# Kernel tuning notes

Measured on AMD Instinct MI355X. Metric: run time of the kernel, lower is better.

Reference implementation:

```python
import jax, jax.numpy as jnp
import numpy as np

B, S, D, H, L, TPB = 4, 1020, 1024, 16, 4, 17
VOBS, VACT = 4096, 16
DH = D // H
EPS = 1e-3  # keras LayerNormalization default epsilon


def _ln(x, g, b):
    m = jnp.mean(x, axis=-1, keepdims=True)
    v = jnp.mean((x - m) ** 2, axis=-1, keepdims=True)
    return (x - m) * jax.lax.rsqrt(v + EPS) * g + b


def setup_inputs() -> dict:
    key = jax.random.key(0)
    ks = iter(jax.random.split(key, 64))
    def p(shape, s=0.02):
        return jax.random.normal(next(ks), shape, jnp.float32) * s
    pos = np.arange(S)
    is_obs = jnp.asarray((pos % TPB) < (TPB - 1))
    tok = jax.random.randint(next(ks), (B, S), 0, VOBS)
    tok = jnp.where(is_obs[None, :], tok, tok % VACT).astype(jnp.int32)
    d = dict(
        tokens=tok,
        pos_emb=p((S, D)), emb_obs=p((VOBS, D)), emb_act=p((VACT, D)),
        ln1_g=jnp.ones((L, D)), ln1_b=jnp.zeros((L, D)),
        wq=p((L, D, D)), bq=jnp.zeros((L, D)),
        wk=p((L, D, D)), bk=jnp.zeros((L, D)),
        wv=p((L, D, D)), bv=jnp.zeros((L, D)),
        wo=p((L, D, D)), bo=jnp.zeros((L, D)),
        ln2_g=jnp.ones((L, D)), ln2_b=jnp.zeros((L, D)),
        w1=p((L, D, 4 * D)), b1=jnp.zeros((L, 4 * D)),
        w2=p((L, 4 * D, D)), b2=jnp.zeros((L, D)),
        lnf_g=jnp.ones((D,)), lnf_b=jnp.zeros((D,)),
        ho1=p((D, D)), bo1=jnp.zeros((D,)),
        ho2=p((D, VOBS)), bo2=jnp.zeros((VOBS,)),
        he1=p((D, D)), be1=jnp.zeros((D,)),
        he2=p((D, 2)), be2=jnp.zeros((2,)),
    )
    return d


def reference(tokens, pos_emb, emb_obs, emb_act, ln1_g, ln1_b, wq, bq, wk, bk,
              wv, bv, wo, bo, ln2_g, ln2_b, w1, b1, w2, b2, lnf_g, lnf_b,
              ho1, bo1, ho2, bo2, he1, be1, he2, be2):
    pos = jnp.arange(S)
    is_obs = (pos % TPB) < (TPB - 1)  # obs positions within each block
    # token embedding: obs table on obs positions, act table on act positions
    x = jnp.where(is_obs[None, :, None],
                  emb_obs[jnp.minimum(tokens, VOBS - 1)],
                  emb_act[jnp.minimum(tokens, VACT - 1)])
    x = x + pos_emb[None]
    neg_mask = (1.0 - jnp.tril(jnp.ones((S, S), jnp.float32))) * -1e9
    inv_sqrt_dk = 1.0 / np.sqrt(DH).astype(np.float32)
    for i in range(L):
        h = _ln(x, ln1_g[i], ln1_b[i])
        q = (h @ wq[i] + bq[i]).reshape(B, S, H, DH).transpose(0, 2, 1, 3)
        k = (h @ wk[i] + bk[i]).reshape(B, S, H, DH).transpose(0, 2, 1, 3)
        v = (h @ wv[i] + bv[i]).reshape(B, S, H, DH).transpose(0, 2, 1, 3)
        scores = jnp.einsum('bhqd,bhkd->bhqk', q, k) * inv_sqrt_dk + neg_mask
        w = jax.nn.softmax(scores, axis=-1)
        o = jnp.einsum('bhqk,bhkd->bhqd', w, v).transpose(0, 2, 1, 3).reshape(B, S, D)
        x = x + (o @ wo[i] + bo[i])
        h = _ln(x, ln2_g[i], ln2_b[i])
        h = jax.nn.gelu(h @ w1[i] + b1[i], approximate=False) @ w2[i] + b2[i]
        x = x + h
    x = _ln(x, lnf_g, lnf_b)
    # head slices (static)
    p_np = np.arange(S)
    head_obs_idx = jnp.asarray(np.nonzero(((p_np + 1) % TPB) != (TPB - 1))[0])  # 960
    act_idx = jnp.asarray(np.nonzero((p_np % TPB) == (TPB - 1))[0])            # 60
    xo = x[:, head_obs_idx]
    logits_obs = jax.nn.relu(xo @ ho1 + bo1) @ ho2 + bo2   # [B, 960, VOBS]
    xe = x[:, act_idx]
    logits_ends = jax.nn.relu(xe @ he1 + be1) @ he2 + be2  # [B, 60, 2]
    return (logits_obs, logits_ends)
```

## Files before the change

kernel.cpp:

```cpp
#include <hip/hip_runtime.h>
#include <hip/hip_bf16.h>
#include <math.h>

namespace {

constexpr int kS = 1020, kD = 1024, kTPB = 17, kDH = 64;
constexpr int kVOBS = 4096, kVACT = 16;
constexpr int kBS = 4080;
constexpr float kEPS = 1e-3f;

typedef float f32x4 __attribute__((ext_vector_type(4)));
typedef __bf16 bfx8 __attribute__((ext_vector_type(8)));
typedef unsigned short u16;
typedef u16 us8 __attribute__((ext_vector_type(8)));
typedef u16 us4 __attribute__((ext_vector_type(4)));

__device__ __forceinline__ float bf2f(u16 u) {
  union { unsigned int i; float f; } v; v.i = (unsigned int)u << 16; return v.f;
}
__device__ __forceinline__ u16 f2bf(float f) {
  union { float f; unsigned int i; } v; v.f = f;
  unsigned int r = v.i + 0x7FFFu + ((v.i >> 16) & 1u);
  return (u16)(r >> 16);
}

__global__ void k_embed(const int* __restrict__ tokens, const float* __restrict__ pos_emb,
                        const float* __restrict__ emb_obs, const float* __restrict__ emb_act,
                        float* __restrict__ x) {
  int bs = blockIdx.x;
  int s = bs % kS;
  int tk = tokens[bs];
  bool obs = (s % kTPB) < (kTPB - 1);
  const float* e;
  if (obs) { int t2 = tk < kVOBS - 1 ? tk : kVOBS - 1; e = emb_obs + (size_t)t2 * kD; }
  else     { int t2 = tk < kVACT - 1 ? tk : kVACT - 1; e = emb_act + (size_t)t2 * kD; }
  int c = threadIdx.x * 4;
  float4 ev = *(const float4*)(e + c);
  float4 pv = *(const float4*)(pos_emb + (size_t)s * kD + c);
  float4 o; o.x = ev.x + pv.x; o.y = ev.y + pv.y; o.z = ev.z + pv.z; o.w = ev.w + pv.w;
  *(float4*)(x + (size_t)bs * kD + c) = o;
}

__global__ void k_pack_bias(const float* __restrict__ bq, const float* __restrict__ bk,
                            const float* __restrict__ bv, float* __restrict__ bqkv) {
  int idx = blockIdx.x * 256 + threadIdx.x;
  int l = idx / 3072, rem = idx % 3072;
  int sel = rem >> 10, cc = rem & 1023;
  const float* src = sel == 0 ? bq : (sel == 1 ? bk : bv);
  bqkv[idx] = src[l * kD + cc];
}

__global__ void k_ln(const float* __restrict__ x, const float* __restrict__ g,
                     const float* __restrict__ b, u16* __restrict__ out) {
  int row = blockIdx.x;
  int t = threadIdx.x;
  const float* xr = x + (size_t)row * kD;
  float4 v = *(const float4*)(xr + t * 4);
  float s1 = v.x + v.y + v.z + v.w;
  float s2 = v.x * v.x + v.y * v.y + v.z * v.z + v.w * v.w;
  #pragma unroll
  for (int m = 32; m; m >>= 1) { s1 += __shfl_xor(s1, m); s2 += __shfl_xor(s2, m); }
  __shared__ float ls1[4], ls2[4];
  int w = t >> 6;
  if ((t & 63) == 0) { ls1[w] = s1; ls2[w] = s2; }
  __syncthreads();
  float S1 = ls1[0] + ls1[1] + ls1[2] + ls1[3];
  float S2 = ls2[0] + ls2[1] + ls2[2] + ls2[3];
  float mean = S1 * (1.0f / kD);
  float var = S2 * (1.0f / kD) - mean * mean;
  float rs = rsqrtf(var + kEPS);
  int c = t * 4;
  float4 gv = *(const float4*)(g + c);
  float4 bv = *(const float4*)(b + c);
  us4 o;
  o[0] = f2bf((v.x - mean) * rs * gv.x + bv.x);
  o[1] = f2bf((v.y - mean) * rs * gv.y + bv.y);
  o[2] = f2bf((v.z - mean) * rs * gv.z + bv.z);
  o[3] = f2bf((v.w - mean) * rs * gv.w + bv.w);
  *(us4*)(out + (size_t)row * kD + c) = o;
}

__global__ void k_transpose(const float* __restrict__ in, u16* __restrict__ out,
                            int R, int C, int ld) {
  __shared__ float tile[32][33];
  int tx = threadIdx.x, ty = threadIdx.y;
  int c0 = blockIdx.x * 32, r0 = blockIdx.y * 32;
  #pragma unroll
  for (int i = 0; i < 4; ++i)
    tile[ty + i * 8][tx] = in[(size_t)(r0 + ty + i * 8) * ld + c0 + tx];
  __syncthreads();
  #pragma unroll
  for (int i = 0; i < 4; ++i)
    out[(size_t)(c0 + ty + i * 8) * R + r0 + tx] = f2bf(tile[tx][ty + i * 8]);
}

struct T4 {
  const float* in0; const float* in1; const float* in2; const float* in3;
  u16* out0; u16* out1; u16* out2; u16* out3;
  int ld;
};
__global__ void k_transpose4(T4 sp) {
  const float* in; u16* out;
  switch (blockIdx.z) {
    case 0:  in = sp.in0; out = sp.out0; break;
    case 1:  in = sp.in1; out = sp.out1; break;
    case 2:  in = sp.in2; out = sp.out2; break;
    default: in = sp.in3; out = sp.out3; break;
  }
  __shared__ float tile[32][33];
  int tx = threadIdx.x, ty = threadIdx.y;
  int c0 = blockIdx.x * 32, r0 = blockIdx.y * 32;
  #pragma unroll
  for (int i = 0; i < 4; ++i)
    tile[ty + i * 8][tx] = in[(size_t)(r0 + ty + i * 8) * sp.ld + c0 + tx];
  __syncthreads();
  #pragma unroll
  for (int i = 0; i < 4; ++i)
    out[(size_t)(c0 + ty + i * 8) * 1024 + r0 + tx] = f2bf(tile[tx][ty + i * 8]);
}

template <int EPI, int BM>
__global__ void __launch_bounds__(256)
k_gemm(const u16* __restrict__ A, const u16* __restrict__ Bt, const float* __restrict__ bias,
       const float* __restrict__ resid, void* __restrict__ out, int M, int N, int K, int ldo) {
  constexpr int MFRAG = BM / 32;
  constexpr int LOADS = BM / 64 + 2;
  __shared__ alignas(16) u16 As[3][BM * 32];
  __shared__ alignas(16) u16 Bs[3][128 * 32];
  int tid = threadIdx.x;
  int m0 = blockIdx.x * BM, n0 = blockIdx.y * 128;
  int lane = tid & 63, wv = tid >> 6;
  int wm = wv >> 1, wn = wv & 1;
  f32x4 acc[MFRAG][4] = {};

  auto stage = [&](int buf, int k0) {
    #pragma unroll
    for (int n = 0; n < BM / 64; ++n) {
      int u = n * 256 + tid;
      int r = u >> 2, ch = u & 3;
      int gr = m0 + r; if (gr >= M) gr = M - 1;
      int cg = ch ^ ((r >> 1) & 3);
      const u16* src = A + (size_t)gr * K + k0 + cg * 8;
      __builtin_amdgcn_global_load_lds(
          (const __attribute__((address_space(1))) unsigned int*)src,
          (__attribute__((address_space(3))) unsigned int*)&As[buf][(n * 256 + wv * 64) * 8],
          16, 0, 0);
    }
    #pragma unroll
    for (int n = 0; n < 2; ++n) {
      int u = n * 256 + tid;
      int r = u >> 2, ch = u & 3;
      int cg = ch ^ ((r >> 1) & 3);
      const u16* src = Bt + (size_t)(n0 + r) * K + k0 + cg * 8;
      __builtin_amdgcn_global_load_lds(
          (const __attribute__((address_space(1))) unsigned int*)src,
          (__attribute__((address_space(3))) unsigned int*)&Bs[buf][(n * 256 + wv * 64) * 8],
          16, 0, 0);
    }
  };

  const int nk = K >> 5;
  stage(0, 0);
  stage(1, 32);
  stage(2, 64);
  for (int t = 0; t < nk; ++t) {
    int cur = t % 3;
    if (t + 2 < nk)
      asm volatile("s_waitcnt vmcnt(%0)" :: "i"(2 * LOADS) : "memory");
    else if (t + 1 < nk)
      asm volatile("s_waitcnt vmcnt(%0)" :: "i"(LOADS) : "memory");
    else
      asm volatile("s_waitcnt vmcnt(0)" ::: "memory");
    __builtin_amdgcn_s_barrier();
    __builtin_amdgcn_sched_barrier(0);

    bfx8 af[MFRAG], bfr[4];
    int ch = lane >> 4;
    #pragma unroll
    for (int mf = 0; mf < MFRAG; ++mf) {
      int row = wm * (BM / 2) + mf * 16 + (lane & 15);
      af[mf] = *(const bfx8*)(&As[cur][row * 32 + ((ch ^ ((row >> 1) & 3)) << 3)]);
    }
    #pragma unroll
    for (int nf = 0; nf < 4; ++nf) {
      int row = wn * 64 + nf * 16 + (lane & 15);
      bfr[nf] = *(const bfx8*)(&Bs[cur][row * 32 + ((ch ^ ((row >> 1) & 3)) << 3)]);
    }
    asm volatile("s_waitcnt lgkmcnt(0)" ::: "memory");
    __builtin_amdgcn_s_barrier();
    __builtin_amdgcn_sched_barrier(0);
    if (t + 3 < nk) stage(cur, (t + 3) << 5);

    #pragma unroll
    for (int mf = 0; mf < MFRAG; ++mf)
      #pragma unroll
      for (int nf = 0; nf < 4; ++nf)
        acc[mf][nf] = __builtin_amdgcn_mfma_f32_16x16x32_bf16(af[mf], bfr[nf], acc[mf][nf], 0, 0, 0);
  }

  #pragma unroll
  for (int mf = 0; mf < MFRAG; ++mf) {
    #pragma unroll
    for (int nf = 0; nf < 4; ++nf) {
      int gcol = n0 + wn * 64 + nf * 16 + (lane & 15);
      float bv = bias ? bias[gcol] : 0.0f;
      #pragma unroll
      for (int r = 0; r < 4; ++r) {
        int grow = m0 + wm * (BM / 2) + mf * 16 + (lane >> 4) * 4 + r;
        if (grow >= M) continue;
        float val = acc[mf][nf][r] + bv;
        size_t off2 = (size_t)grow * ldo + gcol;
        if (EPI == 0) {
          ((u16*)out)[off2] = f2bf(val);
        } else if (EPI == 1) {
          ((u16*)out)[off2] = f2bf(val > 0.f ? val : 0.f);
        } else if (EPI == 2) {
          ((u16*)out)[off2] = f2bf(0.5f * val * (1.f + erff(val * 0.70710678118654752440f)));
        } else if (EPI == 3) {
          ((float*)out)[off2] = resid[off2] + val;
        } else {
          ((float*)out)[off2] = val;
        }
      }
    }
  }
}

__device__ __forceinline__ int swz(int row, int colu16) {
  return (row * 64 + colu16) ^ ((row & 7) << 3) ^ ((row & 24) << 1);
}

__global__ void __launch_bounds__(256)
k_attn(const u16* __restrict__ q, const u16* __restrict__ k, const u16* __restrict__ v,
       u16* __restrict__ o, int ldin) {
  __shared__ u16 Kl[64 * 64];
  __shared__ u16 Vt[64 * 64];
  const int qb = blockIdx.x * 64;
  const int bh = blockIdx.y;
  const int b = bh >> 4, hh = bh & 15;
  const int tid = threadIdx.x;
  const int lane = tid & 63, w = tid >> 6;
  const int g = lane >> 4, c = lane & 15;
  const int q0 = qb + w * 16;
  const size_t base = (size_t)(b * kS) * ldin + hh * kDH;

  bfx8 qf0, qf1;
  {
    int qr = q0 + c; if (qr >= kS) qr = kS - 1;
    const u16* qp = q + base + (size_t)qr * ldin + g * 8;
    qf0 = *(const bfx8*)(qp);
    qf1 = *(const bfx8*)(qp + 32);
  }

  float mst = -1e30f, lsum = 0.f;
  f32x4 ot[4] = {};

  const int ntiles = blockIdx.x + 1;
  for (int t = 0; t < ntiles; ++t) {
    const int kt = t * 64;
    {
      int kr = tid >> 2, ds2 = (tid & 3) * 16;
      int kg = kt + kr; if (kg >= kS) kg = kS - 1;
      const u16* kp = k + base + (size_t)kg * ldin + ds2;
      us8 a0 = *(const us8*)(kp);
      us8 a1 = *(const us8*)(kp + 8);
      *(us8*)(&Kl[swz(kr, ds2)]) = a0;
      *(us8*)(&Kl[swz(kr, ds2 + 8)]) = a1;
      const u16* vp = v + base + (size_t)kg * ldin + ds2;
      us8 b0 = *(const us8*)(vp);
      us8 b1 = *(const us8*)(vp + 8);
      #pragma unroll
      for (int i2 = 0; i2 < 8; ++i2) Vt[swz(ds2 + i2, kr)] = b0[i2];
      #pragma unroll
      for (int i2 = 0; i2 < 8; ++i2) Vt[swz(ds2 + 8 + i2, kr)] = b1[i2];
    }
    __syncthreads();

    f32x4 s[4];
    #pragma unroll
    for (int kb = 0; kb < 4; ++kb) {
      bfx8 kf0 = *(const bfx8*)(&Kl[swz(kb * 16 + c, g * 8)]);
      bfx8 kf1 = *(const bfx8*)(&Kl[swz(kb * 16 + c, g * 8 + 32)]);
      f32x4 acc = {};
      acc = __builtin_amdgcn_mfma_f32_16x16x32_bf16(kf0, qf0, acc, 0, 0, 0);
      acc = __builtin_amdgcn_mfma_f32_16x16x32_bf16(kf1, qf1, acc, 0, 0, 0);
      s[kb] = acc;
    }

    const int qg = q0 + c;
    const bool diag = (kt + 63 > q0);
    float p[4][4];
    float tmax = -1e30f;
    #pragma unroll
    for (int kb = 0; kb < 4; ++kb)
      #pragma unroll
      for (int r = 0; r < 4; ++r) {
        float val = s[kb][r] * 0.125f;
        if (diag && (kt + kb * 16 + g * 4 + r > qg)) val = -1e30f;
        p[kb][r] = val;
        tmax = fmaxf(tmax, val);
      }
    tmax = fmaxf(tmax, __shfl_xor(tmax, 16));
    tmax = fmaxf(tmax, __shfl_xor(tmax, 32));
    float mnew = fmaxf(mst, tmax);
    float alpha = __expf(mst - mnew);
    float psum = 0.f;
    #pragma unroll
    for (int kb = 0; kb < 4; ++kb)
      #pragma unroll
      for (int r = 0; r < 4; ++r) {
        float e = __expf(p[kb][r] - mnew);
        p[kb][r] = e;
        psum += e;
      }
    psum += __shfl_xor(psum, 16);
    psum += __shfl_xor(psum, 32);
    lsum = lsum * alpha + psum;
    mst = mnew;
    #pragma unroll
    for (int db = 0; db < 4; ++db) {
      ot[db][0] *= alpha; ot[db][1] *= alpha;
      ot[db][2] *= alpha; ot[db][3] *= alpha;
    }

    #pragma unroll
    for (int h = 0; h < 2; ++h) {
      bfx8 pf;
      #pragma unroll
      for (int j = 0; j < 8; ++j)
        pf[j] = (__bf16)p[2 * h + (j >> 2)][j & 3];
      #pragma unroll
      for (int db = 0; db < 4; ++db) {
        us4 lo = *(const us4*)(&Vt[swz(16 * db + c, 32 * h + 4 * g)]);
        us4 hi = *(const us4*)(&Vt[swz(16 * db + c, 32 * h + 16 + 4 * g)]);
        union { us8 u; bfx8 bf; } cv;
        cv.u[0] = lo[0]; cv.u[1] = lo[1]; cv.u[2] = lo[2]; cv.u[3] = lo[3];
        cv.u[4] = hi[0]; cv.u[5] = hi[1]; cv.u[6] = hi[2]; cv.u[7] = hi[3];
        ot[db] = __builtin_amdgcn_mfma_f32_16x16x32_bf16(cv.bf, pf, ot[db], 0, 0, 0);
      }
    }
    __syncthreads();
  }

  if (q0 + c < kS) {
    float inv = 1.0f / lsum;
    u16* op = o + (size_t)(b * kS) * kD + hh * kDH + (size_t)(q0 + c) * kD;
    #pragma unroll
    for (int db = 0; db < 4; ++db)
      #pragma unroll
      for (int r = 0; r < 4; ++r)
        op[16 * db + 4 * g + r] = f2bf(ot[db][r] * inv);
  }
}

__global__ void k_gather_obs(const u16* __restrict__ xf, u16* __restrict__ xo) {
  int r = blockIdx.x;
  int b = r / 960, rr = r % 960;
  int j = rr & 15, blk = rr >> 4;
  int s = blk * kTPB + j + (j == 15 ? 1 : 0);
  const unsigned int* src = (const unsigned int*)(xf + ((size_t)(b * kS + s)) * kD);
  unsigned int* dst = (unsigned int*)(xo + (size_t)r * kD);
  dst[threadIdx.x] = src[threadIdx.x];
  dst[threadIdx.x + 256] = src[threadIdx.x + 256];
}
__global__ void k_gather_act(const u16* __restrict__ xf, u16* __restrict__ xe) {
  int r = blockIdx.x;
  int b = r / 60, rr = r % 60;
  int s = rr * kTPB + (kTPB - 1);
  const unsigned int* src = (const unsigned int*)(xf + ((size_t)(b * kS + s)) * kD);
  unsigned int* dst = (unsigned int*)(xe + (size_t)r * kD);
  dst[threadIdx.x] = src[threadIdx.x];
  dst[threadIdx.x + 256] = src[threadIdx.x + 256];
}

__global__ void k_ends(const u16* __restrict__ t2, const float* __restrict__ he2,
                       const float* __restrict__ be2, float* __restrict__ out) {
  int r = blockIdx.x;
  int t = threadIdx.x;
  float p0 = 0.f, p1 = 0.f;
  for (int j = t; j < kD; j += 256) {
    float xv = bf2f(t2[(size_t)r * kD + j]);
    p0 += xv * he2[j * 2];
    p1 += xv * he2[j * 2 + 1];
  }
  #pragma unroll
  for (int msk = 32; msk; msk >>= 1) { p0 += __shfl_xor(p0, msk); p1 += __shfl_xor(p1, msk); }
  __shared__ float l0[4], l1[4];
  int w = t >> 6;
  if ((t & 63) == 0) { l0[w] = p0; l1[w] = p1; }
  __syncthreads();
  if (t == 0) {
    out[r * 2 + 0] = l0[0] + l0[1] + l0[2] + l0[3] + be2[0];
    out[r * 2 + 1] = l1[0] + l1[1] + l1[2] + l1[3] + be2[1];
  }
}

}

extern "C" void kernel_launch(void* const* d_in, const int* in_sizes, int n_in,
                              void* d_out, int out_size, void* d_ws, size_t ws_size,
                              hipStream_t stream) {
  const int*   tokens  = (const int*)  d_in[0];
  const float* pos_emb = (const float*)d_in[1];
  const float* emb_obs = (const float*)d_in[2];
  const float* emb_act = (const float*)d_in[3];
  const float* ln1_g = (const float*)d_in[4];
  const float* ln1_b = (const float*)d_in[5];
  const float* wq = (const float*)d_in[6];
  const float* bq = (const float*)d_in[7];
  const float* wk = (const float*)d_in[8];
  const float* bk = (const float*)d_in[9];
  const float* wv = (const float*)d_in[10];
  const float* bv = (const float*)d_in[11];
  const float* wo = (const float*)d_in[12];
  const float* bo = (const float*)d_in[13];
  const float* ln2_g = (const float*)d_in[14];
  const float* ln2_b = (const float*)d_in[15];
  const float* w1 = (const float*)d_in[16];
  const float* b1 = (const float*)d_in[17];
  const float* w2 = (const float*)d_in[18];
  const float* b2 = (const float*)d_in[19];
  const float* lnf_g = (const float*)d_in[20];
  const float* lnf_b = (const float*)d_in[21];
  const float* ho1 = (const float*)d_in[22];
  const float* bo1 = (const float*)d_in[23];
  const float* ho2 = (const float*)d_in[24];
  const float* bo2 = (const float*)d_in[25];
  const float* he1 = (const float*)d_in[26];
  const float* be1 = (const float*)d_in[27];
  const float* he2 = (const float*)d_in[28];
  const float* be2 = (const float*)d_in[29];
  (void)in_sizes; (void)n_in; (void)out_size; (void)ws_size;

  char* ws = (char*)d_ws;
  size_t off = 0;
  auto alloc = [&](size_t bytes) -> char* {
    char* p = ws + off; off += (bytes + 255) & ~(size_t)255; return p;
  };
  u16*   wTbig = (u16*)alloc((size_t)4096 * 1024 * 2);
  u16*   w2T   = (u16*)alloc((size_t)1024 * 4096 * 2);
  float* x  = (float*)alloc((size_t)kBS * kD * 4);
  u16*   h  = (u16*)alloc((size_t)kBS * kD * 2);
  char*  scr = alloc((size_t)kBS * 4096 * 2);
  float* bqkv = (float*)alloc((size_t)4 * 3072 * 4);
  const size_t slotB = (size_t)kBS * kD * 2;
  u16* qkv = (u16*)scr;
  u16* ob  = (u16*)(scr + (size_t)kBS * 3072 * 2);
  u16* mid = (u16*)scr;
  u16* xf = (u16*)scr;
  u16* xo = (u16*)(scr + slotB);
  u16* t1 = (u16*)(scr + 2 * slotB);
  u16* xe = (u16*)(scr + 3 * slotB);
  u16* t2 = (u16*)(scr + 3 * slotB + (size_t)240 * kD * 2 + 256);

  dim3 tb(32, 8);
  dim3 tg(32, 32);
  k_embed<<<kBS, 256, 0, stream>>>(tokens, pos_emb, emb_obs, emb_act, x);
  k_pack_bias<<<48, 256, 0, stream>>>(bq, bk, bv, bqkv);

  const size_t MB1 = (size_t)1024 * 1024;
  for (int i = 0; i < 4; ++i) {
    const size_t wOff = (size_t)i * kD * kD;
    k_ln<<<kBS, 256, 0, stream>>>(x, ln1_g + i * kD, ln1_b + i * kD, h);

    {
      T4 sp{wq + wOff, wk + wOff, wv + wOff, wo + wOff,
            wTbig, wTbig + MB1, wTbig + 2 * MB1, wTbig + 3 * MB1, 1024};
      k_transpose4<<<dim3(32, 32, 4), tb, 0, stream>>>(sp);
    }
    k_gemm<0, 128><<<dim3(32, 24), 256, 0, stream>>>(h, wTbig, bqkv + i * 3072, nullptr, qkv,
                                                     kBS, 3072, 1024, 3072);

    k_attn<<<dim3(16, 64), 256, 0, stream>>>(qkv, qkv + 1024, qkv + 2048, ob, 3072);

    k_gemm<3, 64><<<dim3(64, 8), 256, 0, stream>>>(ob, wTbig + 3 * MB1, bo + i * kD, x, x,
                                                   kBS, 1024, 1024, 1024);

    k_ln<<<kBS, 256, 0, stream>>>(x, ln2_g + i * kD, ln2_b + i * kD, h);

    {
      const float* w1b = w1 + (size_t)i * kD * 4096;
      T4 sp{w1b, w1b + 1024, w1b + 2048, w1b + 3072,
            wTbig, wTbig + MB1, wTbig + 2 * MB1, wTbig + 3 * MB1, 4096};
      k_transpose4<<<dim3(32, 32, 4), tb, 0, stream>>>(sp);
    }
    k_transpose<<<dim3(32, 128), tb, 0, stream>>>(w2 + (size_t)i * 4096 * kD, w2T,
                                                  4096, 1024, 1024);
    k_gemm<2, 128><<<dim3(32, 32), 256, 0, stream>>>(h, wTbig, b1 + (size_t)i * 4096, nullptr,
                                                     mid, kBS, 4096, 1024, 4096);
    k_gemm<3, 64><<<dim3(64, 8), 256, 0, stream>>>(mid, w2T, b2 + i * kD, x, x,
                                                   kBS, 1024, 4096, 1024);
  }

  k_ln<<<kBS, 256, 0, stream>>>(x, lnf_g, lnf_b, xf);
  k_gather_obs<<<3840, 256, 0, stream>>>(xf, xo);
  k_gather_act<<<240, 256, 0, stream>>>(xf, xe);

  k_transpose<<<tg, tb, 0, stream>>>(ho1, wTbig, 1024, 1024, 1024);
  k_gemm<1, 64><<<dim3(60, 8), 256, 0, stream>>>(xo, wTbig, bo1, nullptr, t1,
                                                 3840, 1024, 1024, 1024);
  k_transpose<<<tg, tb, 0, stream>>>(he1, w2T, 1024, 1024, 1024);
  {
    T4 sp{ho2, ho2 + 1024, ho2 + 2048, ho2 + 3072,
          wTbig, wTbig + MB1, wTbig + 2 * MB1, wTbig + 3 * MB1, 4096};
    k_transpose4<<<dim3(32, 32, 4), tb, 0, stream>>>(sp);
  }
  k_gemm<4, 128><<<dim3(30, 32), 256, 0, stream>>>(t1, wTbig, bo2, nullptr,
                                                   (float*)d_out, 3840, 4096, 1024, 4096);
  k_gemm<1, 64><<<dim3(4, 8), 256, 0, stream>>>(xe, w2T, be1, nullptr, t2,
                                                240, 1024, 1024, 1024);
  k_ends<<<240, 256, 0, stream>>>(t2, he2, be2, (float*)d_out + (size_t)3840 * 4096);
}
```

Measured before the change: 1.283 ms.

## Add 256x256-tile GEMM with direct global-to-LDS loads for wide-N projections

Adds a new 512-thread GEMM kernel that uses 256x256 output tiles and a BK=64 double-buffered pipeline. Tiles are loaded straight into LDS with global_load_lds and an XOR swizzle, and the prefetch loads are interleaved between MFMA phases under setprio. It replaces the QKV, FFN-up and output-head GEMMs, raising arithmetic intensity per tile and cutting register-staged copies. In exchange the grids are much smaller (192-256 blocks on a 256-CU part), so there is a risk of under-filling the GPU and tail imbalance. The new kernel also relies on heavy register and LDS use.

After: 1.266 ms. Within noise of the previous version (-1.3%).

```diff
diff --git a/kernel.cpp b/kernel.cpp
--- a/kernel.cpp
+++ b/kernel.cpp
@@ -117,6 +117,121 @@
   #pragma unroll
   for (int i = 0; i < 4; ++i)
     out[(size_t)(c0 + ty + i * 8) * 1024 + r0 + tx] = f2bf(tile[tx][ty + i * 8]);
+}
+
+template <int EPI>
+__global__ void __launch_bounds__(512, 2)
+k_gemm256(const u16* __restrict__ A, const u16* __restrict__ Bt, const float* __restrict__ bias,
+          void* __restrict__ out, int M, int K, int ldo) {
+  __shared__ alignas(16) u16 As[2][256 * 64];
+  __shared__ alignas(16) u16 Bs[2][256 * 64];
+  const int tid = threadIdx.x;
+  const int lane = tid & 63, wv = tid >> 6;
+  const int wm = wv >> 2, wn = wv & 3;
+  const int m0 = blockIdx.x * 256, n0 = blockIdx.y * 256;
+  f32x4 acc[8][4] = {};
+
+  auto stageIter = [&](int buf, int k0, int it) {
+    int u = (it & 3) * 512 + tid;
+    int row = u >> 3, g = u & 7;
+    int gsw = g ^ (row & 7);
+    int grow;
+    const u16* srcBase;
+    u16* dstBase;
+    if (it < 4) {
+      grow = m0 + row; if (grow >= M) grow = M - 1;
+      srcBase = A; dstBase = &As[buf][0];
+    } else {
+      grow = n0 + row;
+      srcBase = Bt; dstBase = &Bs[buf][0];
+    }
+    const u16* src = srcBase + (size_t)grow * K + k0 + gsw * 8;
+    u16* dst = dstBase + ((it & 3) * 512 + wv * 64) * 8;
+    __builtin_amdgcn_global_load_lds(
+        (const __attribute__((address_space(1))) unsigned int*)src,
+        (__attribute__((address_space(3))) unsigned int*)dst, 16, 0, 0);
+  };
+
+  const int nt = K >> 6;
+  #pragma unroll
+  for (int it = 0; it < 8; ++it) stageIter(0, 0, it);
+
+  for (int t = 0; t < nt; ++t) {
+    const int pb = t & 1;
+    const int k0n = (t + 1) << 6;
+    const bool pf = (t + 1 < nt);
+    asm volatile("s_waitcnt vmcnt(0)" ::: "memory");
+    __builtin_amdgcn_s_barrier();
+    __builtin_amdgcn_sched_barrier(0);
+
+    #pragma unroll
+    for (int kh = 0; kh < 2; ++kh) {
+      bfx8 bfr[4], afr[4];
+      #pragma unroll
+      for (int n = 0; n < 4; ++n) {
+        int row = wn * 64 + n * 16 + (lane & 15);
+        bfr[n] = *(const bfx8*)(&Bs[pb][row * 64 + ((((kh << 2) + (lane >> 4)) ^ (row & 7)) << 3)]);
+      }
+      #pragma unroll
+      for (int j = 0; j < 4; ++j) {
+        int row = wm * 128 + j * 16 + (lane & 15);
+        afr[j] = *(const bfx8*)(&As[pb][row * 64 + ((((kh << 2) + (lane >> 4)) ^ (row & 7)) << 3)]);
+      }
+      if (pf) { stageIter(pb ^ 1, k0n, kh * 4 + 0); stageIter(pb ^ 1, k0n, kh * 4 + 1); }
+      __builtin_amdgcn_s_barrier();
+      asm volatile("s_waitcnt lgkmcnt(0)" ::: "memory");
+      __builtin_amdgcn_sched_barrier(0);
+      __builtin_amdgcn_s_setprio(1);
+      #pragma unroll
+      for (int j = 0; j < 4; ++j)
+        #pragma unroll
+        for (int n = 0; n < 4; ++n)
+          acc[j][n] = __builtin_amdgcn_mfma_f32_16x16x32_bf16(afr[j], bfr[n], acc[j][n], 0, 0, 0);
+      __builtin_amdgcn_s_setprio(0);
+      __builtin_amdgcn_s_barrier();
+
+      #pragma unroll
+      for (int j = 0; j < 4; ++j) {
+        int row = wm * 128 + 64 + j * 16 + (lane & 15);
+        afr[j] = *(const bfx8*)(&As[pb][row * 64 + ((((kh << 2) + (lane >> 4)) ^ (row & 7)) << 3)]);
+      }
+      if (pf) { stageIter(pb ^ 1, k0n, kh * 4 + 2); stageIter(pb ^ 1, k0n, kh * 4 + 3); }
+      __builtin_amdgcn_s_barrier();
+      asm volatile("s_waitcnt lgkmcnt(0)" ::: "memory");
+      __builtin_amdgcn_sched_barrier(0);
+      __builtin_amdgcn_s_setprio(1);
+      #pragma unroll
+      for (int j = 0; j < 4; ++j)
+        #pragma unroll
+        for (int n = 0; n < 4; ++n)
+          acc[4 + j][n] = __builtin_amdgcn_mfma_f32_16x16x32_bf16(afr[j], bfr[n], acc[4 + j][n], 0, 0, 0);
+      __builtin_amdgcn_s_setprio(0);
+      __builtin_amdgcn_s_barrier();
+    }
+  }
+
+  #pragma unroll
+  for (int jf = 0; jf < 8; ++jf) {
+    #pragma unroll
+    for (int n = 0; n < 4; ++n) {
+      int gcol = n0 + wn * 64 + n * 16 + (lane & 15);
+      float bv = bias ? bias[gcol] : 0.0f;
+      #pragma unroll
+      for (int r = 0; r < 4; ++r) {
+        int grow = m0 + wm * 128 + jf * 16 + (lane >> 4) * 4 + r;
+        if (grow >= M) continue;
+        float val = acc[jf][n][r] + bv;
+        size_t o2 = (size_t)grow * ldo + gcol;
+        if (EPI == 0) {
+          ((u16*)out)[o2] = f2bf(val);
+        } else if (EPI == 2) {
+          ((u16*)out)[o2] = f2bf(0.5f * val * (1.f + erff(val * 0.70710678118654752440f)));
+        } else {
+          ((float*)out)[o2] = val;
+        }
+      }
+    }
+  }
 }
 
 template <int EPI, int BM>
@@ -468,8 +583,8 @@
             wTbig, wTbig + MB1, wTbig + 2 * MB1, wTbig + 3 * MB1, 1024};
       k_transpose4<<<dim3(32, 32, 4), tb, 0, stream>>>(sp);
     }
-    k_gemm<0, 128><<<dim3(32, 24), 256, 0, stream>>>(h, wTbig, bqkv + i * 3072, nullptr, qkv,
-                                                     kBS, 3072, 1024, 3072);
+    k_gemm256<0><<<dim3(16, 12), 512, 0, stream>>>(h, wTbig, bqkv + i * 3072, qkv,
+                                                   kBS, 1024, 3072);
 
     k_attn<<<dim3(16, 64), 256, 0, stream>>>(qkv, qkv + 1024, qkv + 2048, ob, 3072);
 
@@ -486,8 +601,8 @@
     }
     k_transpose<<<dim3(32, 128), tb, 0, stream>>>(w2 + (size_t)i * 4096 * kD, w2T,
                                                   4096, 1024, 1024);
-    k_gemm<2, 128><<<dim3(32, 32), 256, 0, stream>>>(h, wTbig, b1 + (size_t)i * 4096, nullptr,
-                                                     mid, kBS, 4096, 1024, 4096);
+    k_gemm256<2><<<dim3(16, 16), 512, 0, stream>>>(h, wTbig, b1 + (size_t)i * 4096,
+                                                   mid, kBS, 1024, 4096);
     k_gemm<3, 64><<<dim3(64, 8), 256, 0, stream>>>(mid, w2T, b2 + i * kD, x, x,
                                                    kBS, 1024, 4096, 1024);
   }
@@ -505,8 +620,8 @@
           wTbig, wTbig + MB1, wTbig + 2 * MB1, wTbig + 3 * MB1, 4096};
     k_transpose4<<<dim3(32, 32, 4), tb, 0, stream>>>(sp);
   }
-  k_gemm<4, 128><<<dim3(30, 32), 256, 0, stream>>>(t1, wTbig, bo2, nullptr,
-                                                   (float*)d_out, 3840, 4096, 1024, 4096);
+  k_gemm256<4><<<dim3(15, 16), 512, 0, stream>>>(t1, wTbig, bo2,
+                                                 (float*)d_out, 3840, 1024, 4096);
   k_gemm<1, 64><<<dim3(4, 8), 256, 0, stream>>>(xe, w2T, be1, nullptr, t2,
                                                 240, 1024, 1024, 1024);
   k_ends<<<240, 256, 0, stream>>>(t2, he2, be2, (float*)d_out + (size_t)3840 * 4096);
```
